# Kernel optimization log

Measured on AMD Instinct MI355X. Metric: run time of the kernel, lower is better.

The kernel has to match this reference:

```python
import jax, jax.numpy as jnp
import numpy as np

N_NODES = 100000
N_EDGES = 600000
NFEAT = 128
HIDDEN = 64
NCLASS = 40


def _sage_conv(x, edge_index, Wl, bl, Wr):
    """PyG SAGEConv with mean aggregation.

    out = lin_l(mean_{j in N(i)} x_j) + lin_r(x_i)
    edge_index[0] = source j, edge_index[1] = target i.
    """
    src, dst = edge_index[0], edge_index[1]
    n = x.shape[0]
    # scatter-mean: sum messages then divide by in-degree (0-degree -> 0)
    msg_sum = jax.ops.segment_sum(x[src], dst, num_segments=n)          # [N, F]
    deg = jax.ops.segment_sum(jnp.ones_like(src, dtype=x.dtype), dst,
                              num_segments=n)                            # [N]
    agg = msg_sum / jnp.maximum(deg, 1.0)[:, None]
    return agg @ Wl + bl + x @ Wr


def setup_inputs() -> dict:
    key = jax.random.key(0)
    ks = jax.random.split(key, 8)
    x = jax.random.normal(ks[0], (N_NODES, NFEAT), dtype=jnp.float32)
    edge_index = jax.random.randint(ks[1], (2, N_EDGES), 0, N_NODES, dtype=jnp.int64)
    s1 = 1.0 / np.sqrt(NFEAT)
    s2 = 1.0 / np.sqrt(HIDDEN)
    return {
        "x": x,
        "edge_index": edge_index,
        "W1l": jax.random.uniform(ks[2], (NFEAT, HIDDEN), jnp.float32, -s1, s1),
        "b1": jnp.zeros((HIDDEN,), jnp.float32),
        "W1r": jax.random.uniform(ks[3], (NFEAT, HIDDEN), jnp.float32, -s1, s1),
        "W2l": jax.random.uniform(ks[4], (HIDDEN, NCLASS), jnp.float32, -s2, s2),
        "b2": jnp.zeros((NCLASS,), jnp.float32),
        "W2r": jax.random.uniform(ks[5], (HIDDEN, NCLASS), jnp.float32, -s2, s2),
    }


def reference(x, edge_index, W1l, b1, W1r, W2l, b2, W2r):
    h = _sage_conv(x, edge_index, W1l, b1, W1r)   # [N, 64]
    h = jax.nn.sigmoid(h)
    out = _sage_conv(h, edge_index, W2l, b2, W2r)  # [N, nclass]
    return out
```

## Files before the change

kernel.cpp:

```cpp
#include <hip/hip_runtime.h>
#include <hip/hip_bf16.h>


#define N_FEAT 128
#define HID 64
#define NCLS 40
#define NE_BLK 4096
#define ECAP 2048

typedef short short8 __attribute__((ext_vector_type(8)));
typedef float floatx4 __attribute__((ext_vector_type(4)));

static __device__ __forceinline__ short f2bf(float x) {
    __hip_bfloat16 h = __float2bfloat16(x);
    return __builtin_bit_cast(short, h);
}
static __device__ __forceinline__ float bf2f(unsigned short u) {
    unsigned int v = ((unsigned int)u) << 16;
    return __builtin_bit_cast(float, v);
}

#define GATHER4(SRC, Zsrc, AC)                                               \
    for (int r = 0; r < d; r += 4) {                                         \
        int i1 = (r + 1 < d) ? r + 1 : d - 1;                                \
        int i2 = (r + 2 < d) ? r + 2 : d - 1;                                \
        int i3 = (r + 3 < d) ? r + 3 : d - 1;                                \
        int j0 = SRC[s + r], j1 = SRC[s + i1];                               \
        int j2 = SRC[s + i2], j3 = SRC[s + i3];                              \
        uint2 v0 = *(const uint2*)(Zsrc + (size_t)j0 * 64 + col * 4);        \
        uint2 v1 = *(const uint2*)(Zsrc + (size_t)j1 * 64 + col * 4);        \
        uint2 v2 = *(const uint2*)(Zsrc + (size_t)j2 * 64 + col * 4);        \
        uint2 v3 = *(const uint2*)(Zsrc + (size_t)j3 * 64 + col * 4);        \
        float w1 = (r + 1 < d) ? 1.f : 0.f;                                  \
        float w2 = (r + 2 < d) ? 1.f : 0.f;                                  \
        float w3 = (r + 3 < d) ? 1.f : 0.f;                                  \
        AC[0] += bf2f((unsigned short)(v0.x & 0xffffu));                     \
        AC[1] += bf2f((unsigned short)(v0.x >> 16));                         \
        AC[2] += bf2f((unsigned short)(v0.y & 0xffffu));                     \
        AC[3] += bf2f((unsigned short)(v0.y >> 16));                         \
        AC[0] = fmaf(w1, bf2f((unsigned short)(v1.x & 0xffffu)), AC[0]);     \
        AC[1] = fmaf(w1, bf2f((unsigned short)(v1.x >> 16)), AC[1]);         \
        AC[2] = fmaf(w1, bf2f((unsigned short)(v1.y & 0xffffu)), AC[2]);     \
        AC[3] = fmaf(w1, bf2f((unsigned short)(v1.y >> 16)), AC[3]);         \
        AC[0] = fmaf(w2, bf2f((unsigned short)(v2.x & 0xffffu)), AC[0]);     \
        AC[1] = fmaf(w2, bf2f((unsigned short)(v2.x >> 16)), AC[1]);         \
        AC[2] = fmaf(w2, bf2f((unsigned short)(v2.y & 0xffffu)), AC[2]);     \
        AC[3] = fmaf(w2, bf2f((unsigned short)(v2.y >> 16)), AC[3]);         \
        AC[0] = fmaf(w3, bf2f((unsigned short)(v3.x & 0xffffu)), AC[0]);     \
        AC[1] = fmaf(w3, bf2f((unsigned short)(v3.x >> 16)), AC[1]);         \
        AC[2] = fmaf(w3, bf2f((unsigned short)(v3.y & 0xffffu)), AC[2]);     \
        AC[3] = fmaf(w3, bf2f((unsigned short)(v3.y >> 16)), AC[3]);         \
    }

#define TILE_SORT()                                                          \
    __syncthreads();                                                         \
    if (t < 64) cnt[t] = 0;                                                  \
    __syncthreads();                                                         \
    for (int j = t; j < cn; j += 256)                                        \
        atomicAdd(&cnt[ebuf[E0 + c0 + j] >> 26], 1);                         \
    __syncthreads();                                                         \
    if (t < 64) {                                                            \
        int v = cnt[t];                                                      \
        int xx = v;                                                          \
        _Pragma("unroll")                                                    \
        for (int o = 1; o < 64; o <<= 1) {                                   \
            int y = __shfl_up(xx, o);                                        \
            if (t >= o) xx += y;                                             \
        }                                                                    \
        pos[t] = xx - v;                       \
    }                                                                        \
    __syncthreads();                                                         \
    for (int j = t; j < cn; j += 256) {                                      \
        unsigned u = ebuf[E0 + c0 + j];                                      \
        int r = atomicAdd(&pos[u >> 26], 1);                                 \
        elist[r] = (int)(u & 0x03FFFFFFu);                                   \
    }                                                                        \
    __syncthreads();

__global__ void prep_hist(const float* __restrict__ W1l, const float* __restrict__ W1r,
                          const float* __restrict__ W2l, const float* __restrict__ W2r,
                          unsigned short* __restrict__ wt1,
                          unsigned short* __restrict__ wt2,
                          int* __restrict__ flags,
                          const int* __restrict__ ei, int ne, int n,
                          int* __restrict__ bh, int nbe) {
    __shared__ int bins[2048];
    const int b = blockIdx.x, t = threadIdx.x;
    const int nbuck = (n + 63) >> 6;
    for (int i = t; i < nbuck; i += 256) bins[i] = 0;
    __syncthreads();
    const int e0 = b * NE_BLK;
    const int lim = (e0 + NE_BLK < ne) ? (e0 + NE_BLK) : ne;
    for (int e = e0 + t; e < lim; e += 256)
        atomicAdd(&bins[ei[ne + e] >> 6], 1);

    int i = b * 256 + t;
    if (i < 128 * 128) {
        int nn = i >> 7, k = i & 127;
        float v = (nn < 64) ? W1l[k * 64 + nn] : W1r[k * 64 + (nn - 64)];
        wt1[nn * 128 + k] = (unsigned short)f2bf(v);
    } else if (i < 128 * 128 + 48 * 128) {
        int j = i - 128 * 128;
        int nn = j >> 7, k = j & 127;
        float v = 0.f;
        if (nn < 40)
            v = (k < 64) ? W2l[k * 40 + nn] : W2r[(k - 64) * 40 + nn];
        wt2[nn * 128 + k] = (unsigned short)f2bf(v);
    }
    if (i < 256) flags[i] = 0;

    __syncthreads();
    for (int j = t; j < nbuck; j += 256) bh[(size_t)j * nbe + b] = bins[j];
}

__global__ void scan_fused(const int* __restrict__ in, int* __restrict__ pre,
                           int m, int* __restrict__ bsums,
                           int* __restrict__ flags) {
    __shared__ int lds[256];
    __shared__ int look[128];
    __shared__ int sprefix;
    const int b = blockIdx.x, t = threadIdx.x;
    const int base = b * 2048 + t * 8;
    int v[8], s = 0;
#pragma unroll
    for (int i = 0; i < 8; ++i) {
        int idx = base + i;
        v[i] = (idx < m) ? in[idx] : 0;
        s += v[i];
    }
    lds[t] = s;
    __syncthreads();
    for (int o = 1; o < 256; o <<= 1) {
        int y = (t >= o) ? lds[t - o] : 0;
        __syncthreads();
        lds[t] += y;
        __syncthreads();
    }
    if (t == 255) {
        __hip_atomic_store(&bsums[b], lds[255], __ATOMIC_RELEASE,
                           __HIP_MEMORY_SCOPE_AGENT);
        __hip_atomic_store(&flags[b], 1, __ATOMIC_RELEASE,
                           __HIP_MEMORY_SCOPE_AGENT);
    }
    if (t < 128) look[t] = 0;
    __syncthreads();
    if (t < b) {
        while (__hip_atomic_load(&flags[t], __ATOMIC_ACQUIRE,
                                 __HIP_MEMORY_SCOPE_AGENT) == 0) {}
        look[t] = __hip_atomic_load(&bsums[t], __ATOMIC_RELAXED,
                                    __HIP_MEMORY_SCOPE_AGENT);
    }
    __syncthreads();
    if (t == 0) {
        int p = 0;
        for (int i = 0; i < b; ++i) p += look[i];
        sprefix = p;
    }
    __syncthreads();
    int run = ((t == 0) ? 0 : lds[t - 1]) + sprefix;
#pragma unroll
    for (int i = 0; i < 8; ++i) {
        run += v[i];
        int idx = base + i;
        if (idx < m) pre[idx + 1] = run;
    }
    if (b == 0 && t == 0) pre[0] = 0;
}

static __device__ __forceinline__ void gemm1_body(
    short* __restrict__ smem, const float* __restrict__ x,
    const unsigned short* __restrict__ Wt, unsigned short* __restrict__ Zl,
    unsigned short* __restrict__ Zr, int n, int bid) {
    constexpr int K = 128, LDA = K + 8, M = 128, MT = 8, KS = 4, QROW = 16;
    short* At = smem;
    short* Bt = smem + 64 * LDA;
    const int t = threadIdx.x;
    const int nodeBase = bid * 64;

    for (int q = t; q < 64 * QROW; q += 256) {
        int row = q / QROW;
        int k0 = (q % QROW) * 8;
        int node = nodeBase + row;
        short8 s = {0, 0, 0, 0, 0, 0, 0, 0};
        if (node < n) {
            const float* A = x + (size_t)node * K + k0;
            float4 v0 = *(const float4*)A;
            float4 v1 = *(const float4*)(A + 4);
            s[0] = f2bf(v0.x); s[1] = f2bf(v0.y);
            s[2] = f2bf(v0.z); s[3] = f2bf(v0.w);
            s[4] = f2bf(v1.x); s[5] = f2bf(v1.y);
            s[6] = f2bf(v1.z); s[7] = f2bf(v1.w);
        }
        *(short8*)&At[row * LDA + k0] = s;
    }
    for (int q = t; q < M * QROW; q += 256) {
        int row = q / QROW;
        int k0 = (q % QROW) * 8;
        *(short8*)&Bt[row * LDA + k0] =
            *(const short8*)((const short*)Wt + (size_t)row * K + k0);
    }
    __syncthreads();

    const int wave = t >> 6;
    const int lane = t & 63;
    const int m0 = wave * 16;
    const int fl = lane & 15;
    const int quad = lane >> 4;

    floatx4 acc[MT];
#pragma unroll
    for (int nt = 0; nt < MT; ++nt) acc[nt] = (floatx4){0.f, 0.f, 0.f, 0.f};

#pragma unroll
    for (int ks = 0; ks < KS; ++ks) {
        const int kb = ks * 32 + quad * 8;
        short8 a = *(const short8*)&At[(m0 + fl) * LDA + kb];
#pragma unroll
        for (int nt = 0; nt < MT; ++nt) {
            short8 b = *(const short8*)&Bt[(nt * 16 + fl) * LDA + kb];
            acc[nt] = __builtin_amdgcn_mfma_f32_16x16x32_bf16(a, b, acc[nt], 0, 0, 0);
        }
    }

#pragma unroll
    for (int nt = 0; nt < MT; ++nt) {
        const int col = nt * 16 + fl;
#pragma unroll
        for (int r = 0; r < 4; ++r) {
            int node = nodeBase + m0 + quad * 4 + r;
            if (node < n) {
                unsigned short v = (unsigned short)f2bf(acc[nt][r]);
                if (col < HID)
                    Zl[(size_t)node * HID + col] = v;
                else
                    Zr[(size_t)node * HID + (col - HID)] = v;
            }
        }
    }
}

__global__ __launch_bounds__(256) void scatter_gemm1(
    const int* __restrict__ ei, int ne, int n, const int* __restrict__ sbase,
    unsigned* __restrict__ ebuf, int nbe, const float* __restrict__ x,
    const unsigned short* __restrict__ wt1, unsigned short* __restrict__ zl,
    unsigned short* __restrict__ zr) {
    __shared__ __align__(16) short smem[(64 + 128) * 136];
    const int b = blockIdx.x;
    if (b < nbe) {
        int* bins = (int*)smem;
        const int t = threadIdx.x;
        const int nbuck = (n + 63) >> 6;
        for (int i = t; i < nbuck; i += 256) bins[i] = 0;
        __syncthreads();
        const int e0 = b * NE_BLK;
        const int lim = (e0 + NE_BLK < ne) ? (e0 + NE_BLK) : ne;
        for (int e = e0 + t; e < lim; e += 256) {
            int d = ei[ne + e];
            int s = ei[e];
            int bk = d >> 6;
            int r = atomicAdd(&bins[bk], 1);
            int p = sbase[(size_t)bk * nbe + b] + r;
            ebuf[p] = ((unsigned)(d & 63) << 26) | (unsigned)s;
        }
    } else {
        gemm1_body(smem, x, wt1, zl, zr, n, b - nbe);
    }
}

__global__ __launch_bounds__(256) void agg_h(
    const unsigned short* __restrict__ Zl, const unsigned short* __restrict__ Zr,
    const unsigned* __restrict__ ebuf, const int* __restrict__ sbase, int nbe,
    const float* __restrict__ bias, unsigned short* __restrict__ hout,
    int* __restrict__ csrO, int* __restrict__ degO, int n) {
    __shared__ int elist[ECAP];
    __shared__ int cnt[64];
    __shared__ int pos[64];
    const int t = threadIdx.x;
    const int tile = blockIdx.x;
    const int base = tile * 64;
    const int E0 = sbase[(size_t)tile * nbe];
    const int E1 = sbase[(size_t)(tile + 1) * nbe];
    const int nedge = E1 - E0;

    const int lane = t & 63, wave = t >> 6;
    const int sub = lane >> 4, col = lane & 15;

    float a[4][4];
    int totd[4];
#pragma unroll
    for (int p = 0; p < 4; ++p) {
        totd[p] = 0;
#pragma unroll
        for (int j = 0; j < 4; ++j) a[p][j] = 0.f;
    }

    for (int c0 = 0; c0 < nedge; c0 += ECAP) {
        const int cn = (nedge - c0 < ECAP) ? (nedge - c0) : ECAP;
        TILE_SORT()
        for (int j = t; j < cn; j += 256) csrO[E0 + c0 + j] = elist[j];
#pragma unroll
        for (int p = 0; p < 4; ++p) {
            const int i = wave * 16 + p * 4 + sub;
            const int s = pos[i] - cnt[i];
            const int d = cnt[i];
            totd[p] += d;
            float* AC = a[p];
            GATHER4(elist, Zl, AC)
        }
    }

#pragma unroll
    for (int p = 0; p < 4; ++p) {
        const int i = wave * 16 + p * 4 + sub;
        const int node = base + i;
        if (node < n) {
            if (col == 0) degO[node] = totd[p];
            float inv = 1.0f / fmaxf((float)totd[p], 1.0f);
            uint2 z = *(const uint2*)(Zr + (size_t)node * 64 + col * 4);
            float4 bb = ((const float4*)bias)[col];
            float r0 = a[p][0] * inv + bf2f((unsigned short)(z.x & 0xffffu)) + bb.x;
            float r1 = a[p][1] * inv + bf2f((unsigned short)(z.x >> 16)) + bb.y;
            float r2 = a[p][2] * inv + bf2f((unsigned short)(z.y & 0xffffu)) + bb.z;
            float r3 = a[p][3] * inv + bf2f((unsigned short)(z.y >> 16)) + bb.w;
            r0 = 1.0f / (1.0f + __expf(-r0));
            r1 = 1.0f / (1.0f + __expf(-r1));
            r2 = 1.0f / (1.0f + __expf(-r2));
            r3 = 1.0f / (1.0f + __expf(-r3));
            uint2 pk;
            pk.x = (unsigned)(unsigned short)f2bf(r0) |
                   ((unsigned)(unsigned short)f2bf(r1) << 16);
            pk.y = (unsigned)(unsigned short)f2bf(r2) |
                   ((unsigned)(unsigned short)f2bf(r3) << 16);
            *(uint2*)(hout + (size_t)node * 64 + col * 4) = pk;
        }
    }
}

__global__ __launch_bounds__(256) void agg_gemm2(
    const unsigned short* __restrict__ h, const unsigned short* __restrict__ Wt,
    const float* __restrict__ bias, const unsigned* __restrict__ ebuf,
    const int* __restrict__ sbase, int nbe, const int* __restrict__ csrI,
    const int* __restrict__ degI, float* __restrict__ out, int n) {
    constexpr int LDA = 136;
    __shared__ __align__(16) short At[64 * LDA];
    __shared__ __align__(16) short Bt[48 * LDA];
    __shared__ int elist[ECAP];
    __shared__ int cnt[64];
    __shared__ int pos[64];
    const int t = threadIdx.x;
    const int tile = blockIdx.x;
    const int base = tile * 64;
    const int E0 = sbase[(size_t)tile * nbe];
    const int E1 = sbase[(size_t)(tile + 1) * nbe];
    const int nedge = E1 - E0;

    for (int q = t; q < 64 * 8; q += 256) {
        int row = q >> 3, k0 = (q & 7) * 8;
        int node = base + row;
        short8 s = {0, 0, 0, 0, 0, 0, 0, 0};
        if (node < n) s = *(const short8*)(h + (size_t)node * 64 + k0);
        *(short8*)&At[row * LDA + 64 + k0] = s;
    }
    for (int q = t; q < 48 * 16; q += 256) {
        int row = q >> 4, k0 = (q & 15) * 8;
        *(short8*)&Bt[row * LDA + k0] =
            *(const short8*)((const short*)Wt + (size_t)row * 128 + k0);
    }

    const int lane = t & 63, wave = t >> 6;
    const int sub = lane >> 4, col = lane & 15;

    float a[4][4];
    int totd[4];
#pragma unroll
    for (int p = 0; p < 4; ++p) {
        totd[p] = 0;
#pragma unroll
        for (int j = 0; j < 4; ++j) a[p][j] = 0.f;
    }

    if (nedge <= ECAP) {
        for (int j = t; j < nedge; j += 256) elist[j] = csrI[E0 + j];
        if (t < 64) {
            int node = base + t;
            int v = (node < n) ? degI[node] : 0;
            cnt[t] = v;
            int xx = v;
#pragma unroll
            for (int o = 1; o < 64; o <<= 1) {
                int y = __shfl_up(xx, o);
                if (t >= o) xx += y;
            }
            pos[t] = xx;
        }
        __syncthreads();
#pragma unroll
        for (int p = 0; p < 4; ++p) {
            const int i = wave * 16 + p * 4 + sub;
            const int s = pos[i] - cnt[i];
            const int d = cnt[i];
            totd[p] = d;
            float* AC = a[p];
            GATHER4(elist, h, AC)
        }
    } else {
        for (int c0 = 0; c0 < nedge; c0 += ECAP) {
            const int cn = (nedge - c0 < ECAP) ? (nedge - c0) : ECAP;
            TILE_SORT()
#pragma unroll
            for (int p = 0; p < 4; ++p) {
                const int i = wave * 16 + p * 4 + sub;
                const int s = pos[i] - cnt[i];
                const int d = cnt[i];
                totd[p] += d;
                float* AC = a[p];
                GATHER4(elist, h, AC)
            }
        }
    }

#pragma unroll
    for (int p = 0; p < 4; ++p) {
        const int i = wave * 16 + p * 4 + sub;
        float inv = 1.0f / fmaxf((float)totd[p], 1.0f);
        uint2 pk;
        pk.x = (unsigned)(unsigned short)f2bf(a[p][0] * inv) |
               ((unsigned)(unsigned short)f2bf(a[p][1] * inv) << 16);
        pk.y = (unsigned)(unsigned short)f2bf(a[p][2] * inv) |
               ((unsigned)(unsigned short)f2bf(a[p][3] * inv) << 16);
        *(uint2*)&At[i * LDA + col * 4] = pk;
    }
    __syncthreads();

    const int m0 = wave * 16;
    const int fl = lane & 15;
    const int quad = lane >> 4;
    floatx4 acc[3];
#pragma unroll
    for (int nt = 0; nt < 3; ++nt) acc[nt] = (floatx4){0.f, 0.f, 0.f, 0.f};
#pragma unroll
    for (int ks = 0; ks < 4; ++ks) {
        const int kb = ks * 32 + quad * 8;
        short8 av = *(const short8*)&At[(m0 + fl) * LDA + kb];
#pragma unroll
        for (int nt = 0; nt < 3; ++nt) {
            short8 bv = *(const short8*)&Bt[(nt * 16 + fl) * LDA + kb];
            acc[nt] = __builtin_amdgcn_mfma_f32_16x16x32_bf16(av, bv, acc[nt], 0, 0, 0);
        }
    }
#pragma unroll
    for (int nt = 0; nt < 3; ++nt) {
        const int col2 = nt * 16 + fl;
        if (col2 < NCLS) {
            float bv = bias[col2];
#pragma unroll
            for (int r = 0; r < 4; ++r) {
                int node = base + m0 + quad * 4 + r;
                if (node < n)
                    out[(size_t)node * NCLS + col2] = acc[nt][r] + bv;
            }
        }
    }
}

extern "C" void kernel_launch(void* const* d_in, const int* in_sizes, int n_in,
                              void* d_out, int out_size, void* d_ws,
                              size_t ws_size, hipStream_t stream) {
    const float* x = (const float*)d_in[0];
    const int* ei = (const int*)d_in[1];
    const float* W1l = (const float*)d_in[2];
    const float* b1 = (const float*)d_in[3];
    const float* W1r = (const float*)d_in[4];
    const float* W2l = (const float*)d_in[5];
    const float* b2 = (const float*)d_in[6];
    const float* W2r = (const float*)d_in[7];
    float* out = (float*)d_out;

    const int n = in_sizes[0] / N_FEAT;
    const int ne = in_sizes[1] / 2;

    const int nbe = (ne + NE_BLK - 1) / NE_BLK;
    const int nbuck = (n + 63) >> 6;
    const int tot = nbuck * nbe;

    unsigned short* zl1 = (unsigned short*)d_ws;
    unsigned short* zr1 = zl1 + (size_t)n * HID;
    unsigned short* h = zr1 + (size_t)n * HID;
    unsigned short* wt1 = h + (size_t)n * HID;
    unsigned short* wt2 = wt1 + 128 * 128;
    unsigned* ebuf = (unsigned*)(wt2 + 48 * 128);
    int* csr = (int*)(ebuf + ne);
    int* deg = csr + ne;
    int* bh = deg + n;
    int* sbase = bh + tot;
    int* bsums = sbase + (tot + 1);
    int* flags = bsums + 256;

    const int gblocks = (n + 63) / 64;
    const int nsb = (tot + 2047) / 2048;

    prep_hist<<<nbe, 256, 0, stream>>>(W1l, W1r, W2l, W2r, wt1, wt2, flags,
                                       ei, ne, n, bh, nbe);
    scan_fused<<<nsb, 256, 0, stream>>>(bh, sbase, tot, bsums, flags);
    scatter_gemm1<<<nbe + gblocks, 256, 0, stream>>>(ei, ne, n, sbase, ebuf,
                                                     nbe, x, wt1, zl1, zr1);
    agg_h<<<gblocks, 256, 0, stream>>>(zl1, zr1, ebuf, sbase, nbe, b1, h, csr,
                                       deg, n);
    agg_gemm2<<<gblocks, 256, 0, stream>>>(h, wt2, b2, ebuf, sbase, nbe, csr,
                                           deg, out, n);
}
```

Baseline: 185.5 us.

## Drop LDS staging in layer-2 aggregation to shrink shared memory and raise occupancy

```diff
diff --git a/kernel.cpp b/kernel.cpp
--- a/kernel.cpp
+++ b/kernel.cpp
@@ -77,6 +77,25 @@
     }                                                                        \
     __syncthreads();
 
+#define TILE_HIST()                                                          \
+    __syncthreads();                                                         \
+    if (t < 64) cnt[t] = 0;                                                  \
+    __syncthreads();                                                         \
+    for (int j = t; j < cn; j += 256)                                        \
+        atomicAdd(&cnt[ebuf[E0 + c0 + j] >> 26], 1);                         \
+    __syncthreads();                                                         \
+    if (t < 64) {                                                            \
+        int v = cnt[t];                                                      \
+        int xx = v;                                                          \
+        _Pragma("unroll")                                                    \
+        for (int o = 1; o < 64; o <<= 1) {                                   \
+            int y = __shfl_up(xx, o);                                        \
+            if (t >= o) xx += y;                                             \
+        }                                                                    \
+        pos[t] = xx;                                      \
+    }                                                                        \
+    __syncthreads();
+
 __global__ void prep_hist(const float* __restrict__ W1l, const float* __restrict__ W1r,
                           const float* __restrict__ W2l, const float* __restrict__ W2r,
                           unsigned short* __restrict__ wt1,
@@ -336,15 +355,15 @@
     }
 }
 
-__global__ __launch_bounds__(256) void agg_gemm2(
+__global__ __launch_bounds__(256, 7) void agg_gemm2(
     const unsigned short* __restrict__ h, const unsigned short* __restrict__ Wt,
     const float* __restrict__ bias, const unsigned* __restrict__ ebuf,
     const int* __restrict__ sbase, int nbe, const int* __restrict__ csrI,
     const int* __restrict__ degI, float* __restrict__ out, int n) {
-    constexpr int LDA = 136;
+    constexpr int LDA = 72;
+    constexpr int LDB = 136;
     __shared__ __align__(16) short At[64 * LDA];
-    __shared__ __align__(16) short Bt[48 * LDA];
-    __shared__ int elist[ECAP];
+    __shared__ __align__(16) short Bt[48 * LDB];
     __shared__ int cnt[64];
     __shared__ int pos[64];
     const int t = threadIdx.x;
@@ -354,21 +373,15 @@
     const int E1 = sbase[(size_t)(tile + 1) * nbe];
     const int nedge = E1 - E0;
 
-    for (int q = t; q < 64 * 8; q += 256) {
-        int row = q >> 3, k0 = (q & 7) * 8;
-        int node = base + row;
-        short8 s = {0, 0, 0, 0, 0, 0, 0, 0};
-        if (node < n) s = *(const short8*)(h + (size_t)node * 64 + k0);
-        *(short8*)&At[row * LDA + 64 + k0] = s;
-    }
     for (int q = t; q < 48 * 16; q += 256) {
         int row = q >> 4, k0 = (q & 15) * 8;
-        *(short8*)&Bt[row * LDA + k0] =
+        *(short8*)&Bt[row * LDB + k0] =
             *(const short8*)((const short*)Wt + (size_t)row * 128 + k0);
     }
 
     const int lane = t & 63, wave = t >> 6;
     const int sub = lane >> 4, col = lane & 15;
+    const int* __restrict__ srcb = csrI + E0;
 
     float a[4][4];
     int totd[4];
@@ -380,7 +393,6 @@
     }
 
     if (nedge <= ECAP) {
-        for (int j = t; j < nedge; j += 256) elist[j] = csrI[E0 + j];
         if (t < 64) {
             int node = base + t;
             int v = (node < n) ? degI[node] : 0;
@@ -401,12 +413,13 @@
             const int d = cnt[i];
             totd[p] = d;
             float* AC = a[p];
-            GATHER4(elist, h, AC)
+            GATHER4(srcb, h, AC)
         }
     } else {
         for (int c0 = 0; c0 < nedge; c0 += ECAP) {
             const int cn = (nedge - c0 < ECAP) ? (nedge - c0) : ECAP;
-            TILE_SORT()
+            TILE_HIST()
+            const int* __restrict__ srcc = csrI + E0 + c0;
 #pragma unroll
             for (int p = 0; p < 4; ++p) {
                 const int i = wave * 16 + p * 4 + sub;
@@ -414,7 +427,7 @@
                 const int d = cnt[i];
                 totd[p] += d;
                 float* AC = a[p];
-                GATHER4(elist, h, AC)
+                GATHER4(srcc, h, AC)
             }
         }
     }
@@ -435,16 +448,21 @@
     const int m0 = wave * 16;
     const int fl = lane & 15;
     const int quad = lane >> 4;
+    const size_t hrow = (size_t)(base + m0 + fl) * 64;
     floatx4 acc[3];
 #pragma unroll
     for (int nt = 0; nt < 3; ++nt) acc[nt] = (floatx4){0.f, 0.f, 0.f, 0.f};
 #pragma unroll
     for (int ks = 0; ks < 4; ++ks) {
         const int kb = ks * 32 + quad * 8;
-        short8 av = *(const short8*)&At[(m0 + fl) * LDA + kb];
+        short8 av;
+        if (ks < 2)
+            av = *(const short8*)&At[(m0 + fl) * LDA + kb];
+        else
+            av = *(const short8*)(h + hrow + (kb - 64));
 #pragma unroll
         for (int nt = 0; nt < 3; ++nt) {
-            short8 bv = *(const short8*)&Bt[(nt * 16 + fl) * LDA + kb];
+            short8 bv = *(const short8*)&Bt[(nt * 16 + fl) * LDB + kb];
             acc[nt] = __builtin_amdgcn_mfma_f32_16x16x32_bf16(av, bv, acc[nt], 0, 0, 0);
         }
     }
```

Result: no change. 185.9 us (+0.2%).
